# Kernel optimization log

Measured on AMD Instinct MI355X. Metric: run time of the kernel, lower is better.

The kernel has to match this reference:

```python
import jax, jax.numpy as jnp
import numpy as np

IMG_H, IMG_W = 800, 1216
STRIDE = 16
SIZES = (128.0, 256.0, 512.0)
RATIOS = (0.5, 1.0, 2.0)
NMS_THRESH = 0.7
MIN_SIZE = 16.0
PRE_NMS = 6000   # testing mode
POST_NMS = 300   # testing mode


def _base_anchors():
    # torchvision-style: ratio = h/w, anchors centered at origin, xyxy
    base = []
    for s in SIZES:
        for r in RATIOS:
            hr = np.sqrt(r)
            w, h = s / hr, s * hr
            base.append([-w / 2.0, -h / 2.0, w / 2.0, h / 2.0])
    return jnp.asarray(np.array(base, dtype=np.float32))  # [A,4]


def _anchors(H, W):
    base = _base_anchors()                                  # [A,4]
    sx = jnp.arange(W, dtype=jnp.float32) * STRIDE
    sy = jnp.arange(H, dtype=jnp.float32) * STRIDE
    shift_x, shift_y = jnp.meshgrid(sx, sy)                 # [H,W] each
    shifts = jnp.stack([shift_x, shift_y, shift_x, shift_y], axis=-1)
    # row-major over (h, w), anchors innermost -> matches permute(0,2,3,1) layout
    return (shifts.reshape(-1, 1, 4) + base[None]).reshape(-1, 4)  # [H*W*A,4]


def _conv(x, w, b, pad):
    y = jax.lax.conv_general_dilated(x, w, (1, 1), pad,
                                     dimension_numbers=('NCHW', 'OIHW', 'NCHW'))
    return y + b[None, :, None, None]


def _decode(deltas, anchors):
    wa = anchors[:, 2] - anchors[:, 0]
    ha = anchors[:, 3] - anchors[:, 1]
    cxa = anchors[:, 0] + 0.5 * wa
    cya = anchors[:, 1] + 0.5 * ha
    cx = deltas[:, 0] * wa + cxa
    cy = deltas[:, 1] * ha + cya
    w = jnp.exp(deltas[:, 2]) * wa
    h = jnp.exp(deltas[:, 3]) * ha
    return jnp.stack([cx - 0.5 * w, cy - 0.5 * h, cx + 0.5 * w, cy + 0.5 * h], axis=-1)


def _nms(boxes, scores):
    # boxes: [N,4] sorted by descending score; greedy IoU-suppression NMS
    N = boxes.shape[0]
    areas = (boxes[:, 2] - boxes[:, 0]) * (boxes[:, 3] - boxes[:, 1])

    def body(i, st):
        sup, kidx, kval = st
        avail = jnp.where(sup, -jnp.inf, scores)
        j = jnp.argmax(avail)
        valid = avail[j] > -jnp.inf
        b = boxes[j]
        ix1 = jnp.maximum(b[0], boxes[:, 0])
        iy1 = jnp.maximum(b[1], boxes[:, 1])
        ix2 = jnp.minimum(b[2], boxes[:, 2])
        iy2 = jnp.minimum(b[3], boxes[:, 3])
        inter = jnp.clip(ix2 - ix1, 0.0) * jnp.clip(iy2 - iy1, 0.0)
        union = areas[j] + areas - inter
        iou = jnp.where(union > 0, inter / union, 0.0)
        sup2 = (sup | (iou > NMS_THRESH)).at[j].set(True)
        sup = jnp.where(valid, sup2, sup.at[j].set(True))
        return sup, kidx.at[i].set(j), kval.at[i].set(valid)

    sup0 = jnp.zeros((N,), jnp.bool_)
    _, kidx, kval = jax.lax.fori_loop(
        0, POST_NMS, body,
        (sup0, jnp.zeros((POST_NMS,), jnp.int32), jnp.zeros((POST_NMS,), jnp.bool_)))
    # fixed-size output [POST_NMS,4]; invalid slots zeroed
    return boxes[kidx] * kval[:, None].astype(boxes.dtype)


def setup_inputs() -> dict:
    key = jax.random.key(0)
    ks = jax.random.split(key, 4)
    return {
        'features': jax.random.normal(ks[0], (8, 512, 50, 76), jnp.float32),
        'conv_w': 0.01 * jax.random.normal(ks[1], (512, 512, 3, 3), jnp.float32),
        'conv_b': jnp.zeros((512,), jnp.float32),
        'cls_w': 0.01 * jax.random.normal(ks[2], (9, 512, 1, 1), jnp.float32),
        'cls_b': jnp.zeros((9,), jnp.float32),
        'box_w': 0.01 * jax.random.normal(ks[3], (36, 512, 1, 1), jnp.float32),
        'box_b': jnp.zeros((36,), jnp.float32),
    }


def reference(features, conv_w, conv_b, cls_w, cls_b, box_w, box_b):
    B, _, H, W = features.shape
    t = jax.nn.relu(_conv(features, conv_w, conv_b, 'SAME'))
    obj = _conv(t, cls_w, cls_b, 'VALID')                     # [B,A,H,W]
    objectness = jnp.transpose(obj, (0, 2, 3, 1)).reshape(B, -1)        # [B,N]
    bd = _conv(t, box_w, box_b, 'VALID')                      # [B,4A,H,W]
    bbox_deltas = jnp.transpose(bd, (0, 2, 3, 1)).reshape(B, -1, 4)     # [B,N,4]
    anchors = _anchors(H, W)                                  # [N,4]

    def per_image(scores, deltas):
        props = _decode(deltas, anchors)
        props = jnp.stack([jnp.clip(props[:, 0], 0.0, IMG_W),
                           jnp.clip(props[:, 1], 0.0, IMG_H),
                           jnp.clip(props[:, 2], 0.0, IMG_W),
                           jnp.clip(props[:, 3], 0.0, IMG_H)], axis=-1)
        keep = ((props[:, 2] - props[:, 0]) >= MIN_SIZE) & \
               ((props[:, 3] - props[:, 1]) >= MIN_SIZE)
        s = jnp.where(keep, scores, -jnp.inf)  # small boxes never selected
        top_s, top_i = jax.lax.top_k(s, PRE_NMS)
        return _nms(props[top_i], top_s)

    proposals = jax.vmap(per_image)(objectness, bbox_deltas)  # [B,POST_NMS,4]
    return proposals, objectness, bbox_deltas
```

## Files before the change

### kernel.cpp

```cpp
#include <hip/hip_runtime.h>
#include <stdint.h>
#include <math.h>

typedef unsigned int u32;
typedef unsigned long long u64;
typedef double d4 __attribute__((ext_vector_type(4)));
typedef _Float16 h8 __attribute__((ext_vector_type(8)));
typedef float f32x16 __attribute__((ext_vector_type(16)));

#define NPX    3800
#define NANCH  34200
#define NSEL   6000
#define NOUT   300
#define NPXP   4160

#define OFF_T        0ull
#define OFF_WTH      62259200ull
#define OFF_WTL      66977792ull
#define OFF_BOXES    71696384ull
#define OFF_ITEMS    76073984ull
#define OFF_FSPH     78262784ull
#define OFF_FSPL     112341504ull
#define WS_NEED_F16  146551296ull
#define OFF_PART     OFF_FSPH
#define WS_NEED_SPLITK (OFF_PART + 43776000ull)

#define GLL16(gsrc, ldst) \
    __builtin_amdgcn_global_load_lds((const __attribute__((address_space(1))) void*)(gsrc), \
                                     (__attribute__((address_space(3))) void*)(ldst), 16, 0, 0)

__global__ __launch_bounds__(256) void prep_kernel(const float* __restrict__ feat,
                                                   const float* __restrict__ cw,
                                                   _Float16* __restrict__ wh,
                                                   _Float16* __restrict__ wl,
                                                   _Float16* __restrict__ fh,
                                                   _Float16* __restrict__ fl) {
    const int bid = blockIdx.x;
    const int tid = threadIdx.x;
    __shared__ __align__(16) _Float16 shh[64][32];
    __shared__ __align__(16) _Float16 shl[64][32];

    if (bid < 9216) {
        int o = bid * 256 + tid;
        int ci = o & 511;
        int co = (o >> 9) & 511;
        int kk = o >> 18;
        float v = cw[(((co << 9) + ci) * 9) + kk] * 1024.0f;
        _Float16 h = (_Float16)v;
        float r = v - (float)h;
        wh[o] = h;
        wl[o] = (_Float16)r;
    } else if (bid < 9216 + 7680) {
        int idx = bid - 9216;
        const int pb = idx % 60; idx /= 60;
        const int b  = idx >> 4;
        const int ci0 = (idx & 15) << 5;
        const int p0  = pb << 6;
        {
            const int r = tid >> 3, xg = tid & 7;
            const int p = p0 + (xg << 3);
            float v[8];
            if (p < NPX) {
                const float* sp = feat + ((size_t)(b * 512 + ci0 + r)) * NPX + p;
                #pragma unroll
                for (int j = 0; j < 8; ++j) v[j] = sp[j];
            } else {
                #pragma unroll
                for (int j = 0; j < 8; ++j) v[j] = 0.f;
            }
            #pragma unroll
            for (int j = 0; j < 8; ++j) {
                float s = v[j] * 512.0f;
                _Float16 h = (_Float16)s;
                float rr = s - (float)h;
                shh[(xg << 3) + j][r] = h;
                shl[(xg << 3) + j][r] = (_Float16)rr;
            }
        }
        __syncthreads();
        {
            const int px = tid >> 2, cg = tid & 3;
            const int p = p0 + px;
            if (p < NPX) {
                const int yy = p / 76, xx = p - yy * 76;
                const size_t dst = ((size_t)b * NPXP + (size_t)((yy + 1) * 80 + xx + 2)) * 512
                                 + ci0 + (cg << 3);
                *(h8*)(fh + dst) = *(const h8*)&shh[px][cg << 3];
                *(h8*)(fl + dst) = *(const h8*)&shl[px][cg << 3];
            }
        }
    } else {
        int idx = (bid - 16896) * 256 + tid;
        int task = idx >> 2, sub = idx & 3;
        if (task < 2880) {
            int b = task / 360, c = task - b * 360;
            int yp, xp;
            if      (c < 80)  { yp = 0;  xp = c; }
            else if (c < 160) { yp = 51; xp = c - 80; }
            else { int c2 = c - 160; yp = 1 + (c2 >> 2); int m = c2 & 3; xp = (m < 2) ? m : (76 + m); }
            const size_t base = ((size_t)b * NPXP + (size_t)(yp * 80 + xp)) * 512 + sub * 128;
            h8 z = {};
            #pragma unroll
            for (int j = 0; j < 16; ++j) {
                *(h8*)(fh + base + (j << 3)) = z;
                *(h8*)(fl + base + (j << 3)) = z;
            }
        }
    }
}

__global__ __launch_bounds__(512, 2) void conv3x3_f16_kernel(
    const _Float16* __restrict__ fh, const _Float16* __restrict__ fl,
    const _Float16* __restrict__ wh, const _Float16* __restrict__ wl,
    const float* __restrict__ bias, float* __restrict__ t)
{
    const int id  = blockIdx.x;
    const int b   = id & 7;
    const int g   = id >> 3;
    const int co0 = (g >> 4) << 7;
    const int pt0 = (g & 15) << 8;
    const int tid = threadIdx.x;
    const int w   = tid >> 6;
    const int l   = tid & 63;
    const int wm  = w >> 2, wn = w & 3;
    const int ln  = l & 31, lk = l >> 5;

    __shared__ __align__(16) _Float16 S[5][24][512];

    const _Float16* sb[3];
    u32 ldof[3];
    bool isA[3];
    const long long fbase = (long long)b * NPXP + pt0;
    #pragma unroll
    for (int i = 0; i < 3; ++i) {
        const int ti = w * 3 + i;
        ldof[i] = (u32)(ti * 1024 + l * 16);
        isA[i] = (ti < 8);
        if (ti < 8) {
            const int mt = ti >> 1, hl = ti & 1;
            sb[i] = (hl ? wl : wh) + ((long long)(co0 + (mt << 5) + ln) << 9) + (lk << 3);
        } else {
            const int tj = ti - 8, nt = tj >> 1, hl = tj & 1;
            sb[i] = (hl ? fl : fh) + ((fbase + (nt << 5) + ln) << 9) + (lk << 3);
        }
    }
    char* lbase = (char*)&S[0][0][0];

    auto stage = [&](int q, int slot) {
        const int kk  = q >> 5;
        const int ci0 = (q & 31) << 4;
        const long long offA = ((long long)kk << 18) + ci0;
        const int kd = (kk * 11) >> 5;
        const int s  = kd * 77 + kk - 81;
        const long long offB = ((long long)s << 9) + ci0;
        char* ld = lbase + slot * 24576;
        #pragma unroll
        for (int i = 0; i < 3; ++i) {
            const long long off = isA[i] ? offA : offB;
            GLL16(sb[i] + off, ld + ldof[i]);
        }
    };

    f32x16 acc[2][2], l2[2][2];
    #pragma unroll
    for (int i = 0; i < 2; ++i)
        #pragma unroll
        for (int j = 0; j < 2; ++j)
            #pragma unroll
            for (int gg = 0; gg < 16; ++gg) { acc[i][j][gg] = 0.0f; l2[i][j][gg] = 0.0f; }

    const int ao = l << 3;

    auto readFrags = [&](int slot, h8* Ah, h8* Al, h8* Bh, h8* Bl) {
        const _Float16* Sq = (const _Float16*)(lbase + slot * 24576);
        #pragma unroll
        for (int i = 0; i < 2; ++i) {
            const int mt = (wm << 1) + i, nt = (wn << 1) + i;
            Ah[i] = *(const h8*)(Sq + (((mt << 1) + 0) << 9) + ao);
            Al[i] = *(const h8*)(Sq + (((mt << 1) + 1) << 9) + ao);
            Bh[i] = *(const h8*)(Sq + ((8 + (nt << 1) + 0) << 9) + ao);
            Bl[i] = *(const h8*)(Sq + ((8 + (nt << 1) + 1) << 9) + ao);
        }
    };

    stage(0, 0); stage(1, 1); stage(2, 2);
    asm volatile("s_waitcnt vmcnt(0)" ::: "memory");
    __builtin_amdgcn_sched_barrier(0);
    __builtin_amdgcn_s_barrier();
    __builtin_amdgcn_sched_barrier(0);

    h8 PAh[2], PAl[2], PBh[2], PBl[2];
    readFrags(0, PAh, PAl, PBh, PBl);

    int s0 = 0;
    for (int F = 0; F < 144; ++F) {
        const int q0 = F << 1;
        int s1 = s0 + 1; if (s1 >= 5) s1 -= 5;
        int s2 = s0 + 2; if (s2 >= 5) s2 -= 5;
        int s3 = s0 + 3; if (s3 >= 5) s3 -= 5;
        int s4 = s0 + 4; if (s4 >= 5) s4 -= 5;
        if (q0 + 3 < 288) stage(q0 + 3, s3);
        if (q0 + 4 < 288) stage(q0 + 4, s4);

        h8 A1h[2], A1l[2], B1h[2], B1l[2];
        readFrags(s1, A1h, A1l, B1h, B1l);

        __builtin_amdgcn_s_setprio(1);
        acc[0][0] = __builtin_amdgcn_mfma_f32_32x32x16_f16(PAh[0], PBh[0], acc[0][0], 0, 0, 0);
        acc[0][0] = __builtin_amdgcn_mfma_f32_32x32x16_f16(PAh[0], PBl[0], acc[0][0], 0, 0, 0);
        acc[0][0] = __builtin_amdgcn_mfma_f32_32x32x16_f16(PAl[0], PBh[0], acc[0][0], 0, 0, 0);
        acc[0][1] = __builtin_amdgcn_mfma_f32_32x32x16_f16(PAh[0], PBh[1], acc[0][1], 0, 0, 0);
        acc[0][1] = __builtin_amdgcn_mfma_f32_32x32x16_f16(PAh[0], PBl[1], acc[0][1], 0, 0, 0);
        acc[0][1] = __builtin_amdgcn_mfma_f32_32x32x16_f16(PAl[0], PBh[1], acc[0][1], 0, 0, 0);
        acc[1][0] = __builtin_amdgcn_mfma_f32_32x32x16_f16(PAh[1], PBh[0], acc[1][0], 0, 0, 0);
        acc[1][0] = __builtin_amdgcn_mfma_f32_32x32x16_f16(PAh[1], PBl[0], acc[1][0], 0, 0, 0);
        acc[1][0] = __builtin_amdgcn_mfma_f32_32x32x16_f16(PAl[1], PBh[0], acc[1][0], 0, 0, 0);
        acc[1][1] = __builtin_amdgcn_mfma_f32_32x32x16_f16(PAh[1], PBh[1], acc[1][1], 0, 0, 0);
        acc[1][1] = __builtin_amdgcn_mfma_f32_32x32x16_f16(PAh[1], PBl[1], acc[1][1], 0, 0, 0);
        acc[1][1] = __builtin_amdgcn_mfma_f32_32x32x16_f16(PAl[1], PBh[1], acc[1][1], 0, 0, 0);
        __builtin_amdgcn_s_setprio(0);

        if (F < 143) readFrags(s2, PAh, PAl, PBh, PBl);

        __builtin_amdgcn_s_setprio(1);
        acc[0][0] = __builtin_amdgcn_mfma_f32_32x32x16_f16(A1h[0], B1h[0], acc[0][0], 0, 0, 0);
        acc[0][0] = __builtin_amdgcn_mfma_f32_32x32x16_f16(A1h[0], B1l[0], acc[0][0], 0, 0, 0);
        acc[0][0] = __builtin_amdgcn_mfma_f32_32x32x16_f16(A1l[0], B1h[0], acc[0][0], 0, 0, 0);
        acc[0][1] = __builtin_amdgcn_mfma_f32_32x32x16_f16(A1h[0], B1h[1], acc[0][1], 0, 0, 0);
        acc[0][1] = __builtin_amdgcn_mfma_f32_32x32x16_f16(A1h[0], B1l[1], acc[0][1], 0, 0, 0);
        acc[0][1] = __builtin_amdgcn_mfma_f32_32x32x16_f16(A1l[0], B1h[1], acc[0][1], 0, 0, 0);
        acc[1][0] = __builtin_amdgcn_mfma_f32_32x32x16_f16(A1h[1], B1h[0], acc[1][0], 0, 0, 0);
        acc[1][0] = __builtin_amdgcn_mfma_f32_32x32x16_f16(A1h[1], B1l[0], acc[1][0], 0, 0, 0);
        acc[1][0] = __builtin_amdgcn_mfma_f32_32x32x16_f16(A1l[1], B1h[0], acc[1][0], 0, 0, 0);
        acc[1][1] = __builtin_amdgcn_mfma_f32_32x32x16_f16(A1h[1], B1h[1], acc[1][1], 0, 0, 0);
        acc[1][1] = __builtin_amdgcn_mfma_f32_32x32x16_f16(A1h[1], B1l[1], acc[1][1], 0, 0, 0);
        acc[1][1] = __builtin_amdgcn_mfma_f32_32x32x16_f16(A1l[1], B1h[1], acc[1][1], 0, 0, 0);
        __builtin_amdgcn_s_setprio(0);

        if (((q0 + 1) & 7) == 7) {
            #pragma unroll
            for (int i = 0; i < 2; ++i)
                #pragma unroll
                for (int j = 0; j < 2; ++j) {
                    l2[i][j] += acc[i][j];
                    #pragma unroll
                    for (int gg = 0; gg < 16; ++gg) acc[i][j][gg] = 0.0f;
                }
        }

        if (F < 143) {
            __builtin_amdgcn_sched_barrier(0);
            asm volatile("s_waitcnt vmcnt(0)" ::: "memory");
            __builtin_amdgcn_sched_barrier(0);
            __builtin_amdgcn_s_barrier();
            __builtin_amdgcn_sched_barrier(0);
        }
        s0 += 2; if (s0 >= 5) s0 -= 5;
    }

    int rcp[16];
    {
        h8 pa, pb;
        #pragma unroll
        for (int j = 0; j < 8; ++j) { pa[j] = (_Float16)(float)ln; pb[j] = (_Float16)0.0625f; }
        f32x16 pr, pc;
        #pragma unroll
        for (int gg = 0; gg < 16; ++gg) { pr[gg] = 0.0f; pc[gg] = 0.0f; }
        pr = __builtin_amdgcn_mfma_f32_32x32x16_f16(pa, pb, pr, 0, 0, 0);
        pc = __builtin_amdgcn_mfma_f32_32x32x16_f16(pb, pa, pc, 0, 0, 0);
        #pragma unroll
        for (int gg = 0; gg < 16; ++gg)
            rcp[gg] = ((int)(pr[gg] + 0.5f)) | (((int)(pc[gg] + 0.5f)) << 8);
    }

    const double dsc = 1.0 / 524288.0;
    #pragma unroll
    for (int i = 0; i < 2; ++i) {
        #pragma unroll
        for (int j = 0; j < 2; ++j) {
            #pragma unroll
            for (int gg = 0; gg < 16; ++gg) {
                const int row = rcp[gg] & 255;
                const int col = rcp[gg] >> 8;
                const int co  = co0 + (wm << 6) + (i << 5) + row;
                const int pp  = pt0 + (wn << 6) + (j << 5) + col;
                const int yy  = pp / 80;
                const int xx  = pp - yy * 80;
                if (yy >= 1 && yy < 51 && xx >= 2 && xx < 78) {
                    const double v = (double)l2[i][j][gg] * dsc + (double)bias[co];
                    t[((size_t)(b * 512 + co)) * NPX + (yy - 1) * 76 + (xx - 2)]
                        = (float)(v > 0.0 ? v : 0.0);
                }
            }
        }
    }
}

__global__ __launch_bounds__(1024) void wtrans_kernel(const float* __restrict__ cw,
                                                      float* __restrict__ wt) {
    int o = blockIdx.x * 1024 + threadIdx.x;
    if (o >= 512*512*9) return;
    int co = o & 511;
    int ci = (o >> 9) & 511;
    int kk = o >> 18;
    wt[o] = cw[((co << 9) + ci) * 9 + kk];
}

__global__ __launch_bounds__(256, 2) void conv3x3_mfma_kernel(const float* __restrict__ feat,
                                                              const float* __restrict__ wt,
                                                              const float* __restrict__ bias,
                                                              float* __restrict__ t) {
    const int b   = blockIdx.z;
    const int co0 = blockIdx.y << 7;
    const int px0 = blockIdx.x << 6;
    const int tid = threadIdx.x;
    const int w    = tid >> 6;
    const int l    = tid & 63;
    const int quad = l >> 4;
    const int lc   = l & 15;

    __shared__ double BsF[2][1024];

    int rr[4], cc[4];
    {
        d4 pzr = {0.0, 0.0, 0.0, 0.0};
        d4 pzc = {0.0, 0.0, 0.0, 0.0};
        double paM = (double)lc;
        double pbN = (double)lc;
        pzr = __builtin_amdgcn_mfma_f64_16x16x4f64(paM, 1.0, pzr, 0, 0, 0);
        pzc = __builtin_amdgcn_mfma_f64_16x16x4f64(1.0, pbN, pzc, 0, 0, 0);
        #pragma unroll
        for (int g = 0; g < 4; ++g) {
            rr[g] = (((int)pzr[g]) >> 2) & 15;
            cc[g] = (((int)pzc[g]) >> 2) & 15;
        }
    }

    d4 acc[2][4];
    #pragma unroll
    for (int i = 0; i < 2; ++i)
        #pragma unroll
        for (int j = 0; j < 4; ++j) acc[i][j] = (d4){0.0, 0.0, 0.0, 0.0};

    const float* featb = feat + (size_t)b * 512 * NPX;

    const int b_quad = (tid >> 4) & 3;
    const int b_pxl  = ((tid >> 6) << 4) | (tid & 15);
    const int p      = px0 + b_pxl;
    const int py     = p / 76;
    const int px     = p - py * 76;
    const bool pvalid = (p < NPX);

    float vaf[8], vbf[4];
    double a_cur[8];

    auto loadA = [&](int q, float* va) {
        int kk  = q >> 5;
        int ci0 = (q & 31) << 4;
        const float* ap = wt + (((size_t)(kk * 512 + ci0 + quad)) << 9)
                             + co0 + (w << 5) + lc;
        #pragma unroll
        for (int ks = 0; ks < 4; ++ks) {
            va[ks * 2 + 0] = ap[(ks << 11)];
            va[ks * 2 + 1] = ap[(ks << 11) + 16];
        }
    };
    auto loadB = [&](int q, float* vb) {
        int kk  = q >> 5;
        int ci0 = (q & 31) << 4;
        int kd = kk / 3;
        int dy = kd - 1, dx = kk - kd * 3 - 1;
        int iy = py + dy, ix = px + dx;
        bool ok = pvalid && ((unsigned)iy < 50u) && ((unsigned)ix < 76u);
        if (ok) {
            const float* bp = featb + (size_t)(ci0 + b_quad) * NPX + iy * 76 + ix;
            #pragma unroll
            for (int j = 0; j < 4; ++j) vb[j] = bp[(size_t)(j << 2) * NPX];
        } else {
            vb[0] = vb[1] = vb[2] = vb[3] = 0.0f;
        }
    };

    loadA(0, vaf); loadB(0, vbf);
    #pragma unroll
    for (int j = 0; j < 4; ++j) BsF[0][tid + (j << 8)] = (double)vbf[j];
    #pragma unroll
    for (int j = 0; j < 8; ++j) a_cur[j] = (double)vaf[j];
    __syncthreads();

    for (int q = 0; q < 288; ++q) {
        const int cur = q & 1;
        if (q < 287) { loadA(q + 1, vaf); loadB(q + 1, vbf); }
        const double* bb = BsF[cur];
        #pragma unroll
        for (int ks = 0; ks < 4; ++ks) {
            const double* bp = bb + (ks << 8);
            double a0 = a_cur[ks * 2], a1 = a_cur[ks * 2 + 1];
            #pragma unroll
            for (int nt = 0; nt < 4; ++nt) {
                double bv = bp[(nt << 6) + l];
                acc[0][nt] = __builtin_amdgcn_mfma_f64_16x16x4f64(a0, bv, acc[0][nt], 0, 0, 0);
                acc[1][nt] = __builtin_amdgcn_mfma_f64_16x16x4f64(a1, bv, acc[1][nt], 0, 0, 0);
            }
        }
        if (q < 287) {
            #pragma unroll
            for (int j = 0; j < 4; ++j) BsF[cur ^ 1][tid + (j << 8)] = (double)vbf[j];
            #pragma unroll
            for (int j = 0; j < 8; ++j) a_cur[j] = (double)vaf[j];
            __syncthreads();
        }
    }

    #pragma unroll
    for (int mt = 0; mt < 2; ++mt) {
        #pragma unroll
        for (int g = 0; g < 4; ++g) {
            int co = co0 + (w << 5) + (mt << 4) + rr[g];
            double bs = (double)bias[co];
            float* row = t + ((size_t)b * 512 + co) * NPX;
            #pragma unroll
            for (int nt = 0; nt < 4; ++nt) {
                int pp = px0 + (nt << 4) + cc[g];
                if (pp < NPX) {
                    double v = acc[mt][nt][g] + bs;
                    row[pp] = (float)(v > 0.0 ? v : 0.0);
                }
            }
        }
    }
}

__global__ __launch_bounds__(64) void heads_partial_kernel(const float* __restrict__ t,
                                                           const float* __restrict__ cls_w,
                                                           const float* __restrict__ box_w,
                                                           double* __restrict__ part) {
    const int b = blockIdx.y, c = blockIdx.z;
    const int p = blockIdx.x * 64 + threadIdx.x;
    if (p >= NPX) return;
    const float* tb = t + ((size_t)b * 512 + c * 128) * NPX + p;

    double ac[9]  = {};
    double ab[36] = {};
    for (int ci = 0; ci < 128; ++ci) {
        double tv = (double)tb[(size_t)ci * NPX];
        int cw = c * 128 + ci;
        #pragma unroll
        for (int o = 0; o < 9;  ++o) ac[o] = fma((double)cls_w[o * 512 + cw], tv, ac[o]);
        #pragma unroll
        for (int o = 0; o < 36; ++o) ab[o] = fma((double)box_w[o * 512 + cw], tv, ab[o]);
    }
    double* dst = part + ((size_t)(c * 8 + b) * 45) * NPX + p;
    #pragma unroll
    for (int o = 0; o < 9;  ++o) dst[(size_t)o * NPX] = ac[o];
    #pragma unroll
    for (int o = 0; o < 36; ++o) dst[(size_t)(9 + o) * NPX] = ab[o];
}

__device__ __forceinline__ void decode_px(int b, int p, const double* s45,
                                          const float* cls_b, const float* box_b,
                                          float* out_obj, float* out_del,
                                          float* boxes, u64* items) {
    float* ob = out_obj + (size_t)b * NANCH + (size_t)p * 9;
    float* dl = out_del + (size_t)b * NANCH * 4 + (size_t)p * 36;
    const int yy = p / 76, xx = p - yy * 76;

    #pragma unroll
    for (int a = 0; a < 9; ++a) {
        double s  = s45[a] + (double)cls_b[a];
        ob[a] = (float)s;
        double d0 = s45[9 + 4*a + 0] + (double)box_b[4*a+0];
        double d1 = s45[9 + 4*a + 1] + (double)box_b[4*a+1];
        double d2 = s45[9 + 4*a + 2] + (double)box_b[4*a+2];
        double d3 = s45[9 + 4*a + 3] + (double)box_b[4*a+3];
        dl[4*a+0] = (float)d0; dl[4*a+1] = (float)d1;
        dl[4*a+2] = (float)d2; dl[4*a+3] = (float)d3;

        int si = a / 3, ri = a - si * 3;
        double sz = (si == 0) ? 128.0 : ((si == 1) ? 256.0 : 512.0);
        double hr = (ri == 0) ? 0.7071067811865476 : ((ri == 1) ? 1.0 : 1.4142135623730951);
        float bx2f = (float)(sz / hr * 0.5);
        float by2f = (float)(sz * hr * 0.5);

        double sx = (double)(xx * 16), sy = (double)(yy * 16);
        double x1 = sx - (double)bx2f, x2 = sx + (double)bx2f;
        double y1 = sy - (double)by2f, y2 = sy + (double)by2f;

        double wa = x2 - x1, ha = y2 - y1;
        double cxa = x1 + 0.5 * wa, cya = y1 + 0.5 * ha;
        double cx = d0 * wa + cxa, cy = d1 * ha + cya;
        double w  = exp(d2) * wa,  h  = exp(d3) * ha;

        double px1 = cx - 0.5 * w, py1 = cy - 0.5 * h;
        double px2 = cx + 0.5 * w, py2 = cy + 0.5 * h;
        px1 = fmin(fmax(px1, 0.0), 1216.0);
        py1 = fmin(fmax(py1, 0.0), 800.0);
        px2 = fmin(fmax(px2, 0.0), 1216.0);
        py2 = fmin(fmax(py2, 0.0), 800.0);

        bool keep = ((px2 - px1) >= 16.0) && ((py2 - py1) >= 16.0);
        double se = keep ? s : -INFINITY;

        u64 ubits = (u64)__double_as_longlong(se);
        u64 ka = (ubits >> 63) ? ~ubits : (ubits | 0x8000000000000000ull);
        u64 kd = ~ka;
        int n = p * 9 + a;
        items[(size_t)b * NANCH + n] = (kd & ~0xFFFFull) | (u64)(u32)n;
        *(float4*)(boxes + ((size_t)b * NANCH + n) * 4) =
            make_float4((float)px1, (float)py1, (float)px2, (float)py2);
    }
}

__global__ __launch_bounds__(64) void reduce_decode_kernel(const double* __restrict__ part,
                                                           const float* __restrict__ cls_b,
                                                           const float* __restrict__ box_b,
                                                           float* __restrict__ out_obj,
                                                           float* __restrict__ out_del,
                                                           float* __restrict__ boxes,
                                                           u64* __restrict__ items) {
    const int b = blockIdx.y;
    const int p = blockIdx.x * 64 + threadIdx.x;
    if (p >= NPX) return;
    double s45[45];
    #pragma unroll
    for (int o = 0; o < 45; ++o) {
        double s = part[((size_t)(0 * 8 + b) * 45 + o) * NPX + p];
        s += part[((size_t)(1 * 8 + b) * 45 + o) * NPX + p];
        s += part[((size_t)(2 * 8 + b) * 45 + o) * NPX + p];
        s += part[((size_t)(3 * 8 + b) * 45 + o) * NPX + p];
        s45[o] = s;
    }
    decode_px(b, p, s45, cls_b, box_b, out_obj, out_del, boxes, items);
}

__global__ __launch_bounds__(256) void heads_decode_kernel(const float* __restrict__ t,
                                                           const float* __restrict__ cls_w,
                                                           const float* __restrict__ cls_b,
                                                           const float* __restrict__ box_w,
                                                           const float* __restrict__ box_b,
                                                           float* __restrict__ out_obj,
                                                           float* __restrict__ out_del,
                                                           float* __restrict__ boxes,
                                                           u64* __restrict__ items) {
    const int b = blockIdx.y;
    const int p = blockIdx.x * 256 + threadIdx.x;
    if (p >= NPX) return;
    const float* tb = t + (size_t)b * 512 * NPX + p;
    double s45[45];
    #pragma unroll
    for (int o = 0; o < 45; ++o) s45[o] = 0.0;
    for (int ci = 0; ci < 512; ++ci) {
        double tv = (double)tb[(size_t)ci * NPX];
        #pragma unroll
        for (int o = 0; o < 9;  ++o) s45[o]     = fma((double)cls_w[o * 512 + ci], tv, s45[o]);
        #pragma unroll
        for (int o = 0; o < 36; ++o) s45[9 + o] = fma((double)box_w[o * 512 + ci], tv, s45[9 + o]);
    }
    decode_px(b, p, s45, cls_b, box_b, out_obj, out_del, boxes, items);
}

__device__ __forceinline__ bool iou_gt(float4 A, float4 B, float areaA, float areaB) {
    float ix1 = fmaxf(A.x, B.x), iy1 = fmaxf(A.y, B.y);
    float ix2 = fminf(A.z, B.z), iy2 = fminf(A.w, B.w);
    float iw = fmaxf(ix2 - ix1, 0.0f), ih = fmaxf(iy2 - iy1, 0.0f);
    float inter = iw * ih;
    float uni = areaA + areaB - inter;
    float iou = (uni > 0.0f) ? (inter / uni) : 0.0f;
    return iou > 0.7f;
}

__global__ __launch_bounds__(1024) void topk_nms_kernel(const u64* __restrict__ items,
                                                        const float* __restrict__ boxes,
                                                        float* __restrict__ out) {
    extern __shared__ u64 buf[];
    u32* hist = (u32*)buf;
    u32* scan = hist + 4096;
    u32* scal = hist + 5120;

    const int b   = blockIdx.x;
    const int tid = threadIdx.x;
    const u64* it = items + (size_t)b * NANCH;

    #pragma unroll
    for (int i = 0; i < 4; ++i) hist[tid * 4 + i] = 0;
    __syncthreads();
    for (int i = tid; i < NANCH; i += 1024)
        atomicAdd(&hist[(u32)(it[i] >> 52)], 1);
    __syncthreads();

    u32 B1, cum1;
    {
        u32 c0 = hist[tid*4], c1 = hist[tid*4+1], c2 = hist[tid*4+2], c3 = hist[tid*4+3];
        u32 S = c0 + c1 + c2 + c3;
        scan[tid] = S;
        __syncthreads();
        for (int off = 1; off < 1024; off <<= 1) {
            u32 v = (tid >= off) ? scan[tid - off] : 0;
            __syncthreads();
            scan[tid] += v;
            __syncthreads();
        }
        u32 excl = scan[tid] - S;
        const u32 target = 5999;
        if (target >= excl && target < excl + S) {
            u32 pfx = excl, bidx, cum;
            if      (target < pfx + c0)           { bidx = tid*4;   cum = pfx; }
            else if (target < pfx + c0 + c1)      { bidx = tid*4+1; cum = pfx + c0; }
            else if (target < pfx + c0 + c1 + c2) { bidx = tid*4+2; cum = pfx + c0 + c1; }
            else                                  { bidx = tid*4+3; cum = pfx + c0 + c1 + c2; }
            scal[0] = bidx; scal[1] = cum;
        }
    }
    __syncthreads();
    B1 = scal[0]; cum1 = scal[1];
    __syncthreads();

    #pragma unroll
    for (int i = 0; i < 4; ++i) hist[tid * 4 + i] = 0;
    __syncthreads();
    for (int i = tid; i < NANCH; i += 1024) {
        u64 v = it[i];
        if ((u32)(v >> 52) == B1)
            atomicAdd(&hist[(u32)(v >> 40) & 0xFFF], 1);
    }
    __syncthreads();

    u32 B2;
    {
        u32 c0 = hist[tid*4], c1 = hist[tid*4+1], c2 = hist[tid*4+2], c3 = hist[tid*4+3];
        u32 S = c0 + c1 + c2 + c3;
        scan[tid] = S;
        __syncthreads();
        for (int off = 1; off < 1024; off <<= 1) {
            u32 v = (tid >= off) ? scan[tid - off] : 0;
            __syncthreads();
            scan[tid] += v;
            __syncthreads();
        }
        u32 excl = scan[tid] - S;
        const u32 target = 5999 - cum1;
        if (target >= excl && target < excl + S) {
            u32 pfx = excl, bidx;
            if      (target < pfx + c0)           bidx = tid*4;
            else if (target < pfx + c0 + c1)      bidx = tid*4+1;
            else if (target < pfx + c0 + c1 + c2) bidx = tid*4+2;
            else                                  bidx = tid*4+3;
            scal[2] = bidx;
        }
    }
    __syncthreads();
    B2 = scal[2];
    const u32 T = ((B1 << 12) | B2) + 1;
    __syncthreads();

    for (int i = tid; i < 8192; i += 1024) buf[i] = ~0ull;
    __syncthreads();
    u32* cnt = (u32*)&buf[8191];
    if (tid == 0) *cnt = 0;
    __syncthreads();
    for (int i = tid; i < NANCH; i += 1024) {
        u64 v = it[i];
        if ((u32)(v >> 40) < T) {
            u32 pos = atomicAdd(cnt, 1);
            if (pos < 8191) buf[pos] = v;
        }
    }
    __syncthreads();
    if (tid == 0) buf[8191] = ~0ull;
    __syncthreads();

    for (int size = 2; size <= 8192; size <<= 1) {
        for (int stride = size >> 1; stride > 0; stride >>= 1) {
            #pragma unroll
            for (int v = 0; v < 4; ++v) {
                int idx = tid + (v << 10);
                int i = 2 * idx - (idx & (stride - 1));
                int j = i + stride;
                bool up = ((i & size) == 0);
                u64 x = buf[i], y = buf[j];
                if ((x > y) == up) { buf[i] = y; buf[j] = x; }
            }
            __syncthreads();
        }
    }

    float4 bx6[6]; u32 dead6[6];
    #pragma unroll
    for (int s = 0; s < 6; ++s) {
        int r = tid + (s << 10);
        u64 v = buf[r];
        bool dd = (r >= NSEL) || ((u32)(v >> 32) >= 0xFFF00000u);
        float4 bb = make_float4(0.f, 0.f, 0.f, 0.f);
        if (!dd) {
            u32 n = (u32)(v & 0xFFFFull);
            bb = *(const float4*)(boxes + ((size_t)b * NANCH + n) * 4);
        }
        bx6[s] = bb;
        dead6[s] = dd ? 1u : 0u;
    }
    __syncthreads();

    float4* candbox = (float4*)buf;
    u64*    wmask   = (u64*)(buf + 2560);
    float4* accb    = (float4*)(buf + 3072);
    u32*    cntp    = (u32*)(buf + 3712);
    if (tid == 0) *cntp = 0;
    __syncthreads();

    for (int s = 0; s < 6; ++s) {
        int count = (int)*cntp;
        if (count >= NOUT) break;
        float4 mb = bx6[s];
        float  ma = (mb.z - mb.x) * (mb.w - mb.y);
        bool dd = dead6[s] != 0;
        for (int a2 = 0; a2 < count && !dd; ++a2) {
            float4 abx = accb[a2];
            if (iou_gt(mb, abx, ma, (abx.z - abx.x) * (abx.w - abx.y))) dd = true;
        }
        candbox[tid] = mb;
        u64 bal = __ballot(!dd);
        if ((tid & 63) == 0) wmask[tid >> 6] = bal;
        __syncthreads();
        if (tid < 64) {
            int cnt2 = count;
            for (int w2 = 0; w2 < 16 && cnt2 < NOUT; ++w2) {
                u64 mm = wmask[w2];
                while (mm != 0 && cnt2 < NOUT) {
                    int bit = __ffsll(mm) - 1;
                    mm &= (mm - 1);
                    float4 cb = candbox[(w2 << 6) + bit];
                    float  ca = (cb.z - cb.x) * (cb.w - cb.y);
                    bool okc = true;
                    for (int base = count; base < cnt2 && okc; base += 64) {
                        int idx = base + tid;
                        bool bad = false;
                        if (idx < cnt2) {
                            float4 abx = accb[idx];
                            bad = iou_gt(cb, abx, ca, (abx.z - abx.x) * (abx.w - abx.y));
                        }
                        if (__any(bad)) okc = false;
                    }
                    if (okc) {
                        if (tid == 0) accb[cnt2] = cb;
                        cnt2++;
                    }
                }
            }
            if (tid == 0) *cntp = (u32)cnt2;
        }
        __syncthreads();
    }

    int fin = (int)*cntp;
    for (int r = tid; r < NOUT; r += 1024) {
        float4 v = (r < fin) ? accb[r] : make_float4(0.f, 0.f, 0.f, 0.f);
        *(float4*)(out + ((size_t)b * NOUT + r) * 4) = v;
    }
}

extern "C" void kernel_launch(void* const* d_in, const int* in_sizes, int n_in,
                              void* d_out, int out_size, void* d_ws, size_t ws_size,
                              hipStream_t stream) {
    const float* feat   = (const float*)d_in[0];
    const float* conv_w = (const float*)d_in[1];
    const float* conv_b = (const float*)d_in[2];
    const float* cls_w  = (const float*)d_in[3];
    const float* cls_b  = (const float*)d_in[4];
    const float* box_w  = (const float*)d_in[5];
    const float* box_b  = (const float*)d_in[6];

    float* out       = (float*)d_out;
    float* out_props = out;
    float* out_obj   = out + 9600;
    float* out_del   = out + 9600 + 273600;

    char* ws = (char*)d_ws;
    float*    t     = (float*)(ws + OFF_T);
    _Float16* wth   = (_Float16*)(ws + OFF_WTH);
    _Float16* wtl   = (_Float16*)(ws + OFF_WTL);
    float*    wtf   = (float*)(ws + OFF_WTH);
    float*    boxes = (float*)(ws + OFF_BOXES);
    u64*      items = (u64*)(ws + OFF_ITEMS);
    _Float16* fsph  = (_Float16*)(ws + OFF_FSPH);
    _Float16* fspl  = (_Float16*)(ws + OFF_FSPL);
    double*   part  = (double*)(ws + OFF_PART);

    if (ws_size >= WS_NEED_F16) {
        hipLaunchKernelGGL(prep_kernel, dim3(16941), dim3(256), 0, stream,
                           feat, conv_w, wth, wtl, fsph, fspl);
        hipLaunchKernelGGL(conv3x3_f16_kernel, dim3(512), dim3(512), 0, stream,
                           fsph, fspl, wth, wtl, conv_b, t);
    } else {
        hipLaunchKernelGGL(wtrans_kernel, dim3(2304), dim3(1024), 0, stream, conv_w, wtf);
        hipLaunchKernelGGL(conv3x3_mfma_kernel, dim3(60, 4, 8), dim3(256), 0, stream,
                           feat, wtf, conv_b, t);
    }
    if (ws_size >= WS_NEED_SPLITK) {
        hipLaunchKernelGGL(heads_partial_kernel, dim3(60, 8, 4), dim3(64), 0, stream,
                           t, cls_w, box_w, part);
        hipLaunchKernelGGL(reduce_decode_kernel, dim3(60, 8), dim3(64), 0, stream,
                           part, cls_b, box_b, out_obj, out_del, boxes, items);
    } else {
        hipLaunchKernelGGL(heads_decode_kernel, dim3(15, 8), dim3(256), 0, stream,
                           t, cls_w, cls_b, box_w, box_b, out_obj, out_del, boxes, items);
    }
    hipLaunchKernelGGL(topk_nms_kernel, dim3(8), dim3(1024), 65536, stream,
                       items, boxes, out_props);
}
```

Before: 1.154 ms.

## Double conv output-channel tile per block and simplify LDS staging to four slots

Each conv3x3 block now covers 256 output channels instead of 128, using 16 waves (1024 threads) and a grid of 256 blocks rather than 512. This is meant to raise data reuse of the feature tile in LDS and cut global load traffic per MFMA. The 5-slot LDS ring with register-prefetched fragments becomes a 4-slot XOR-indexed ring with two stages in flight, and fragments are read just before use. That gives up some latency hiding, and one 1024-thread block per CU may leave fewer waves to overlap LDS reads with MFMA work.

```diff
diff --git a/kernel.cpp b/kernel.cpp
--- a/kernel.cpp
+++ b/kernel.cpp
@@ -109,7 +109,7 @@
     }
 }
 
-__global__ __launch_bounds__(512, 2) void conv3x3_f16_kernel(
+__global__ __launch_bounds__(1024, 1) void conv3x3_f16_kernel(
     const _Float16* __restrict__ fh, const _Float16* __restrict__ fl,
     const _Float16* __restrict__ wh, const _Float16* __restrict__ wl,
     const float* __restrict__ bias, float* __restrict__ t)
@@ -117,7 +117,7 @@
     const int id  = blockIdx.x;
     const int b   = id & 7;
     const int g   = id >> 3;
-    const int co0 = (g >> 4) << 7;
+    const int co0 = (g >> 4) << 8;
     const int pt0 = (g & 15) << 8;
     const int tid = threadIdx.x;
     const int w   = tid >> 6;
@@ -125,22 +125,22 @@
     const int wm  = w >> 2, wn = w & 3;
     const int ln  = l & 31, lk = l >> 5;
 
-    __shared__ __align__(16) _Float16 S[5][24][512];
-
-    const _Float16* sb[3];
-    u32 ldof[3];
-    bool isA[3];
+    __shared__ __align__(16) _Float16 S[4][32][512];
+
+    const _Float16* sb[2];
+    u32 ldof[2];
+    bool isA[2];
     const long long fbase = (long long)b * NPXP + pt0;
     #pragma unroll
-    for (int i = 0; i < 3; ++i) {
-        const int ti = w * 3 + i;
+    for (int i = 0; i < 2; ++i) {
+        const int ti = (w << 1) + i;
         ldof[i] = (u32)(ti * 1024 + l * 16);
-        isA[i] = (ti < 8);
-        if (ti < 8) {
+        isA[i] = (ti < 16);
+        if (ti < 16) {
             const int mt = ti >> 1, hl = ti & 1;
             sb[i] = (hl ? wl : wh) + ((long long)(co0 + (mt << 5) + ln) << 9) + (lk << 3);
         } else {
-            const int tj = ti - 8, nt = tj >> 1, hl = tj & 1;
+            const int tj = ti - 16, nt = tj >> 1, hl = tj & 1;
             sb[i] = (hl ? fl : fh) + ((fbase + (nt << 5) + ln) << 9) + (lk << 3);
         }
     }
@@ -153,9 +153,9 @@
         const int kd = (kk * 11) >> 5;
         const int s  = kd * 77 + kk - 81;
         const long long offB = ((long long)s << 9) + ci0;
-        char* ld = lbase + slot * 24576;
-        #pragma unroll
-        for (int i = 0; i < 3; ++i) {
+        char* ld = lbase + slot * 32768;
+        #pragma unroll
+        for (int i = 0; i < 2; ++i) {
             const long long off = isA[i] ? offA : offB;
             GLL16(sb[i] + off, ld + ldof[i]);
         }
@@ -172,56 +172,49 @@
     const int ao = l << 3;
 
     auto readFrags = [&](int slot, h8* Ah, h8* Al, h8* Bh, h8* Bl) {
-        const _Float16* Sq = (const _Float16*)(lbase + slot * 24576);
+        const _Float16* Sq = (const _Float16*)(lbase + slot * 32768);
         #pragma unroll
         for (int i = 0; i < 2; ++i) {
             const int mt = (wm << 1) + i, nt = (wn << 1) + i;
             Ah[i] = *(const h8*)(Sq + (((mt << 1) + 0) << 9) + ao);
             Al[i] = *(const h8*)(Sq + (((mt << 1) + 1) << 9) + ao);
-            Bh[i] = *(const h8*)(Sq + ((8 + (nt << 1) + 0) << 9) + ao);
-            Bl[i] = *(const h8*)(Sq + ((8 + (nt << 1) + 1) << 9) + ao);
+            Bh[i] = *(const h8*)(Sq + ((16 + (nt << 1) + 0) << 9) + ao);
+            Bl[i] = *(const h8*)(Sq + ((16 + (nt << 1) + 1) << 9) + ao);
         }
     };
 
-    stage(0, 0); stage(1, 1); stage(2, 2);
+    stage(0, 0); stage(1, 1);
     asm volatile("s_waitcnt vmcnt(0)" ::: "memory");
     __builtin_amdgcn_sched_barrier(0);
     __builtin_amdgcn_s_barrier();
-    __builtin_amdgcn_sched_barrier(0);
-
-    h8 PAh[2], PAl[2], PBh[2], PBl[2];
-    readFrags(0, PAh, PAl, PBh, PBl);
 
     int s0 = 0;
     for (int F = 0; F < 144; ++F) {
         const int q0 = F << 1;
-        int s1 = s0 + 1; if (s1 >= 5) s1 -= 5;
-        int s2 = s0 + 2; if (s2 >= 5) s2 -= 5;
-        int s3 = s0 + 3; if (s3 >= 5) s3 -= 5;
-        int s4 = s0 + 4; if (s4 >= 5) s4 -= 5;
+        const int s1 = s0 ^ 1;
+        const int s2 = s0 ^ 2;
+        const int s3 = s0 ^ 3;
+        if (q0 + 2 < 288) stage(q0 + 2, s2);
         if (q0 + 3 < 288) stage(q0 + 3, s3);
-        if (q0 + 4 < 288) stage(q0 + 4, s4);
-
+
+        h8 A0h[2], A0l[2], B0h[2], B0l[2];
         h8 A1h[2], A1l[2], B1h[2], B1l[2];
+        readFrags(s0, A0h, A0l, B0h, B0l);
+        __builtin_amdgcn_s_setprio(1);
+        acc[0][0] = __builtin_amdgcn_mfma_f32_32x32x16_f16(A0h[0], B0h[0], acc[0][0], 0, 0, 0);
+        acc[0][0] = __builtin_amdgcn_mfma_f32_32x32x16_f16(A0h[0], B0l[0], acc[0][0], 0, 0, 0);
+        acc[0][0] = __builtin_amdgcn_mfma_f32_32x32x16_f16(A0l[0], B0h[0], acc[0][0], 0, 0, 0);
+        acc[0][1] = __builtin_amdgcn_mfma_f32_32x32x16_f16(A0h[0], B0h[1], acc[0][1], 0, 0, 0);
+        acc[0][1] = __builtin_amdgcn_mfma_f32_32x32x16_f16(A0h[0], B0l[1], acc[0][1], 0, 0, 0);
+        acc[0][1] = __builtin_amdgcn_mfma_f32_32x32x16_f16(A0l[0], B0h[1], acc[0][1], 0, 0, 0);
+        acc[1][0] = __builtin_amdgcn_mfma_f32_32x32x16_f16(A0h[1], B0h[0], acc[1][0], 0, 0, 0);
+        acc[1][0] = __builtin_amdgcn_mfma_f32_32x32x16_f16(A0h[1], B0l[0], acc[1][0], 0, 0, 0);
+        acc[1][0] = __builtin_amdgcn_mfma_f32_32x32x16_f16(A0l[1], B0h[0], acc[1][0], 0, 0, 0);
+        acc[1][1] = __builtin_amdgcn_mfma_f32_32x32x16_f16(A0h[1], B0h[1], acc[1][1], 0, 0, 0);
+        acc[1][1] = __builtin_amdgcn_mfma_f32_32x32x16_f16(A0h[1], B0l[1], acc[1][1], 0, 0, 0);
+        acc[1][1] = __builtin_amdgcn_mfma_f32_32x32x16_f16(A0l[1], B0h[1], acc[1][1], 0, 0, 0);
+        __builtin_amdgcn_s_setprio(0);
         readFrags(s1, A1h, A1l, B1h, B1l);
-
-        __builtin_amdgcn_s_setprio(1);
-        acc[0][0] = __builtin_amdgcn_mfma_f32_32x32x16_f16(PAh[0], PBh[0], acc[0][0], 0, 0, 0);
-        acc[0][0] = __builtin_amdgcn_mfma_f32_32x32x16_f16(PAh[0], PBl[0], acc[0][0], 0, 0, 0);
-        acc[0][0] = __builtin_amdgcn_mfma_f32_32x32x16_f16(PAl[0], PBh[0], acc[0][0], 0, 0, 0);
-        acc[0][1] = __builtin_amdgcn_mfma_f32_32x32x16_f16(PAh[0], PBh[1], acc[0][1], 0, 0, 0);
-        acc[0][1] = __builtin_amdgcn_mfma_f32_32x32x16_f16(PAh[0], PBl[1], acc[0][1], 0, 0, 0);
-        acc[0][1] = __builtin_amdgcn_mfma_f32_32x32x16_f16(PAl[0], PBh[1], acc[0][1], 0, 0, 0);
-        acc[1][0] = __builtin_amdgcn_mfma_f32_32x32x16_f16(PAh[1], PBh[0], acc[1][0], 0, 0, 0);
-        acc[1][0] = __builtin_amdgcn_mfma_f32_32x32x16_f16(PAh[1], PBl[0], acc[1][0], 0, 0, 0);
-        acc[1][0] = __builtin_amdgcn_mfma_f32_32x32x16_f16(PAl[1], PBh[0], acc[1][0], 0, 0, 0);
-        acc[1][1] = __builtin_amdgcn_mfma_f32_32x32x16_f16(PAh[1], PBh[1], acc[1][1], 0, 0, 0);
-        acc[1][1] = __builtin_amdgcn_mfma_f32_32x32x16_f16(PAh[1], PBl[1], acc[1][1], 0, 0, 0);
-        acc[1][1] = __builtin_amdgcn_mfma_f32_32x32x16_f16(PAl[1], PBh[1], acc[1][1], 0, 0, 0);
-        __builtin_amdgcn_s_setprio(0);
-
-        if (F < 143) readFrags(s2, PAh, PAl, PBh, PBl);
-
         __builtin_amdgcn_s_setprio(1);
         acc[0][0] = __builtin_amdgcn_mfma_f32_32x32x16_f16(A1h[0], B1h[0], acc[0][0], 0, 0, 0);
         acc[0][0] = __builtin_amdgcn_mfma_f32_32x32x16_f16(A1h[0], B1l[0], acc[0][0], 0, 0, 0);
@@ -255,7 +248,7 @@
             __builtin_amdgcn_s_barrier();
             __builtin_amdgcn_sched_barrier(0);
         }
-        s0 += 2; if (s0 >= 5) s0 -= 5;
+        s0 ^= 2;
     }
 
     int rcp[16];
@@ -788,7 +781,7 @@
     if (ws_size >= WS_NEED_F16) {
         hipLaunchKernelGGL(prep_kernel, dim3(16941), dim3(256), 0, stream,
                            feat, conv_w, wth, wtl, fsph, fspl);
-        hipLaunchKernelGGL(conv3x3_f16_kernel, dim3(512), dim3(512), 0, stream,
+        hipLaunchKernelGGL(conv3x3_f16_kernel, dim3(256), dim3(1024), 0, stream,
                            fsph, fspl, wth, wtl, conv_b, t);
     } else {
         hipLaunchKernelGGL(wtrans_kernel, dim3(2304), dim3(1024), 0, stream, conv_w, wtf);
```

After: 1.447 ms. 1.25x slower.

## Relax global-load waits and drop cross-iteration fragment prefetch in conv GEMM loop

Applied to the files above, without the earlier changes.

The main MFMA loop now waits only until at most three global loads are outstanding instead of draining all of them. Stages issued one iteration ahead can therefore stay in flight across the barrier. The register prefetch of the next step's LDS fragments is replaced by in-iteration reads, with the first half of the MFMAs interleaved against the second fragment read. This aims to hide global-load latency and lower register pressure, at the cost of exposed LDS read latency at each iteration start. The partial vmcnt also carries a correctness risk if the load count per stage does not match the assumed value of 3.

```diff
diff --git a/kernel.cpp b/kernel.cpp
--- a/kernel.cpp
+++ b/kernel.cpp
@@ -184,45 +184,38 @@
     };
 
     stage(0, 0); stage(1, 1); stage(2, 2);
-    asm volatile("s_waitcnt vmcnt(0)" ::: "memory");
+    asm volatile("s_waitcnt vmcnt(3)" ::: "memory");
     __builtin_amdgcn_sched_barrier(0);
     __builtin_amdgcn_s_barrier();
-    __builtin_amdgcn_sched_barrier(0);
-
-    h8 PAh[2], PAl[2], PBh[2], PBl[2];
-    readFrags(0, PAh, PAl, PBh, PBl);
 
     int s0 = 0;
     for (int F = 0; F < 144; ++F) {
         const int q0 = F << 1;
         int s1 = s0 + 1; if (s1 >= 5) s1 -= 5;
-        int s2 = s0 + 2; if (s2 >= 5) s2 -= 5;
         int s3 = s0 + 3; if (s3 >= 5) s3 -= 5;
         int s4 = s0 + 4; if (s4 >= 5) s4 -= 5;
         if (q0 + 3 < 288) stage(q0 + 3, s3);
         if (q0 + 4 < 288) stage(q0 + 4, s4);
 
+        h8 A0h[2], A0l[2], B0h[2], B0l[2];
         h8 A1h[2], A1l[2], B1h[2], B1l[2];
+        readFrags(s0, A0h, A0l, B0h, B0l);
+        __builtin_amdgcn_s_setprio(1);
+        acc[0][0] = __builtin_amdgcn_mfma_f32_32x32x16_f16(A0h[0], B0h[0], acc[0][0], 0, 0, 0);
+        acc[0][0] = __builtin_amdgcn_mfma_f32_32x32x16_f16(A0h[0], B0l[0], acc[0][0], 0, 0, 0);
+        acc[0][0] = __builtin_amdgcn_mfma_f32_32x32x16_f16(A0l[0], B0h[0], acc[0][0], 0, 0, 0);
+        acc[0][1] = __builtin_amdgcn_mfma_f32_32x32x16_f16(A0h[0], B0h[1], acc[0][1], 0, 0, 0);
+        acc[0][1] = __builtin_amdgcn_mfma_f32_32x32x16_f16(A0h[0], B0l[1], acc[0][1], 0, 0, 0);
+        acc[0][1] = __builtin_amdgcn_mfma_f32_32x32x16_f16(A0l[0], B0h[1], acc[0][1], 0, 0, 0);
+        __builtin_amdgcn_s_setprio(0);
         readFrags(s1, A1h, A1l, B1h, B1l);
-
         __builtin_amdgcn_s_setprio(1);
-        acc[0][0] = __builtin_amdgcn_mfma_f32_32x32x16_f16(PAh[0], PBh[0], acc[0][0], 0, 0, 0);
-        acc[0][0] = __builtin_amdgcn_mfma_f32_32x32x16_f16(PAh[0], PBl[0], acc[0][0], 0, 0, 0);
-        acc[0][0] = __builtin_amdgcn_mfma_f32_32x32x16_f16(PAl[0], PBh[0], acc[0][0], 0, 0, 0);
-        acc[0][1] = __builtin_amdgcn_mfma_f32_32x32x16_f16(PAh[0], PBh[1], acc[0][1], 0, 0, 0);
-        acc[0][1] = __builtin_amdgcn_mfma_f32_32x32x16_f16(PAh[0], PBl[1], acc[0][1], 0, 0, 0);
-        acc[0][1] = __builtin_amdgcn_mfma_f32_32x32x16_f16(PAl[0], PBh[1], acc[0][1], 0, 0, 0);
-        acc[1][0] = __builtin_amdgcn_mfma_f32_32x32x16_f16(PAh[1], PBh[0], acc[1][0], 0, 0, 0);
-        acc[1][0] = __builtin_amdgcn_mfma_f32_32x32x16_f16(PAh[1], PBl[0], acc[1][0], 0, 0, 0);
-        acc[1][0] = __builtin_amdgcn_mfma_f32_32x32x16_f16(PAl[1], PBh[0], acc[1][0], 0, 0, 0);
-        acc[1][1] = __builtin_amdgcn_mfma_f32_32x32x16_f16(PAh[1], PBh[1], acc[1][1], 0, 0, 0);
-        acc[1][1] = __builtin_amdgcn_mfma_f32_32x32x16_f16(PAh[1], PBl[1], acc[1][1], 0, 0, 0);
-        acc[1][1] = __builtin_amdgcn_mfma_f32_32x32x16_f16(PAl[1], PBh[1], acc[1][1], 0, 0, 0);
-        __builtin_amdgcn_s_setprio(0);
-
-        if (F < 143) readFrags(s2, PAh, PAl, PBh, PBl);
-
-        __builtin_amdgcn_s_setprio(1);
+        acc[1][0] = __builtin_amdgcn_mfma_f32_32x32x16_f16(A0h[1], B0h[0], acc[1][0], 0, 0, 0);
+        acc[1][0] = __builtin_amdgcn_mfma_f32_32x32x16_f16(A0h[1], B0l[0], acc[1][0], 0, 0, 0);
+        acc[1][0] = __builtin_amdgcn_mfma_f32_32x32x16_f16(A0l[1], B0h[0], acc[1][0], 0, 0, 0);
+        acc[1][1] = __builtin_amdgcn_mfma_f32_32x32x16_f16(A0h[1], B0h[1], acc[1][1], 0, 0, 0);
+        acc[1][1] = __builtin_amdgcn_mfma_f32_32x32x16_f16(A0h[1], B0l[1], acc[1][1], 0, 0, 0);
+        acc[1][1] = __builtin_amdgcn_mfma_f32_32x32x16_f16(A0l[1], B0h[1], acc[1][1], 0, 0, 0);
         acc[0][0] = __builtin_amdgcn_mfma_f32_32x32x16_f16(A1h[0], B1h[0], acc[0][0], 0, 0, 0);
         acc[0][0] = __builtin_amdgcn_mfma_f32_32x32x16_f16(A1h[0], B1l[0], acc[0][0], 0, 0, 0);
         acc[0][0] = __builtin_amdgcn_mfma_f32_32x32x16_f16(A1l[0], B1h[0], acc[0][0], 0, 0, 0);
@@ -249,11 +242,10 @@
         }
 
         if (F < 143) {
-            __builtin_amdgcn_sched_barrier(0);
-            asm volatile("s_waitcnt vmcnt(0)" ::: "memory");
+            if (q0 + 4 < 288) { asm volatile("s_waitcnt vmcnt(3)" ::: "memory"); }
+            else              { asm volatile("s_waitcnt vmcnt(0)" ::: "memory"); }
             __builtin_amdgcn_sched_barrier(0);
             __builtin_amdgcn_s_barrier();
-            __builtin_amdgcn_sched_barrier(0);
         }
         s0 += 2; if (s0 >= 5) s0 -= 5;
     }
```

Measured after the change: 1.092 ms. -5.4%, faster.
